# Kernel tuning notes

Measured on AMD Instinct MI355X. Metric: run time of the kernel, lower is better.

The kernel has to match this reference:

```python
import jax, jax.numpy as jnp
import numpy as np

L2_REG = 0.01  # config['l2_reg']


def setup_inputs() -> dict:
    key = jax.random.key(0)
    k1, k2, k3, k4 = jax.random.split(key, 4)
    N = 16384
    risk_pred = jax.random.normal(k1, (N, 1), dtype=jnp.float32)
    y = jax.random.uniform(k2, (N, 1), dtype=jnp.float32)  # survival times
    e = jax.random.randint(k3, (N, 1), 0, 2, dtype=jnp.int32)  # event indicator
    W = jax.random.normal(k4, (512, 256), dtype=jnp.float32)  # model weight for L2 reg
    return {"risk_pred": risk_pred, "y": y, "e": e, "W": W}


def reference(risk_pred, y, e, W):
    # mask[i, j] = 1 if y[j] <= y[i] else 0  (torch: mask[y.T - y > 0] = 0)
    mask = (y.T - y <= 0).astype(risk_pred.dtype)  # (N, N)
    exp_r = jnp.exp(risk_pred)                      # (N, 1), broadcasts over rows
    num = jnp.sum(exp_r * mask, axis=0)             # (N,) risk-set weighted sum per column
    den = jnp.sum(mask, axis=0)                     # (N,) risk-set size per column
    log_loss = jnp.log(num / den).reshape(-1, 1)    # (N, 1)
    ef = e.astype(risk_pred.dtype)
    neg_log_loss = -jnp.sum((risk_pred - log_loss) * ef) / jnp.sum(ef)
    l2_loss = L2_REG * jnp.linalg.norm(W)           # Regularization(order=2)
    return neg_log_loss + l2_loss
```

## Files before the change

kernel.cpp:

```cpp
#include <hip/hip_runtime.h>

#define L2_REG 0.01f
#define NTOT 16384
#define K    8
#define NBL  4096
#define GB   (K * NBL)
#define CAP  3072
#define NT   1024


__global__ __launch_bounds__(NT) void cox_sort(const float* __restrict__ rp,
                                               const float* __restrict__ y,
                                               const int* __restrict__ e,
                                               const float* __restrict__ W,
                                               float2* __restrict__ g_ye,
                                               int* __restrict__ pub_n,
                                               float* __restrict__ pub_S,
                                               float* __restrict__ pub_w,
                                               float* __restrict__ acc,
                                               int* __restrict__ cnt2) {
    __shared__ __align__(16) float2 s_ye[CAP];
    __shared__ __align__(16) int    s_off[NBL];
    __shared__ int   s_isc[16];
    __shared__ float s_f1[16], s_f2[16];

    const int t = threadIdx.x, wg = blockIdx.x;
    const int lane = t & 63, wave = t >> 6;

    *reinterpret_cast<int4*>(&s_off[4 * t]) = make_int4(0, 0, 0, 0);

    float yv[16], rk[16];
    {
        const float4* y4 = reinterpret_cast<const float4*>(y);
        const float4* r4 = reinterpret_cast<const float4*>(rp);
        const int4*   e4 = reinterpret_cast<const int4*>(e);
#pragma unroll
        for (int k = 0; k < 4; ++k) {
            const float4 yy = y4[k * NT + t];
            const float4 rr = r4[k * NT + t];
            const int4   ee = e4[k * NT + t];
            yv[4*k+0] = yy.x; yv[4*k+1] = yy.y; yv[4*k+2] = yy.z; yv[4*k+3] = yy.w;
            rk[4*k+0] = __int_as_float((__float_as_int(rr.x) & ~1) | (ee.x & 1));
            rk[4*k+1] = __int_as_float((__float_as_int(rr.y) & ~1) | (ee.y & 1));
            rk[4*k+2] = __int_as_float((__float_as_int(rr.z) & ~1) | (ee.z & 1));
            rk[4*k+3] = __int_as_float((__float_as_int(rr.w) & ~1) | (ee.w & 1));
        }
    }
    float wsum = 0.f;
    {
        const float4* W4 = reinterpret_cast<const float4*>(W) + wg * 4096;
#pragma unroll
        for (int m = 0; m < 4; ++m) {
            const float4 w = W4[m * NT + t];
            wsum = fmaf(w.x, w.x, wsum); wsum = fmaf(w.y, w.y, wsum);
            wsum = fmaf(w.z, w.z, wsum); wsum = fmaf(w.w, w.w, wsum);
        }
    }
    __syncthreads();

    const int lo = wg * NBL;
    float sp = 0.f;
#pragma unroll
    for (int k = 0; k < 16; ++k) {
        int g = (int)(yv[k] * (float)GB);
        g = min(max(g, 0), GB - 1);
        const unsigned lb = (unsigned)(g - lo);
        if (lb < NBL) { atomicAdd(&s_off[lb], 1); sp += __expf(rk[k]); }
    }
#pragma unroll
    for (int o = 32; o; o >>= 1) {
        sp   += __shfl_down(sp,   o, 64);
        wsum += __shfl_down(wsum, o, 64);
    }
    if (lane == 0) { s_f1[wave] = sp; s_f2[wave] = wsum; }
    __syncthreads();

    const int4 c4 = *reinterpret_cast<const int4*>(&s_off[4 * t]);
    const int cs = c4.x + c4.y + c4.z + c4.w;
    int ci = cs;
#pragma unroll
    for (int o = 1; o < 64; o <<= 1) {
        const int p = __shfl_up(ci, o, 64);
        if (lane >= o) ci += p;
    }
    if (lane == 63) s_isc[wave] = ci;
    __syncthreads();
    if (t < 16) {
        int v = s_isc[t];
#pragma unroll
        for (int o = 1; o < 16; o <<= 1) {
            const int p = __shfl_up(v, o, 64);
            if (lane >= o) v += p;
        }
        s_isc[t] = v;
    }
    __syncthreads();
    {
        const int base = ci - cs + (wave ? s_isc[wave - 1] : 0);
        s_off[4*t+0] = base;
        s_off[4*t+1] = base + c4.x;
        s_off[4*t+2] = base + c4.x + c4.y;
        s_off[4*t+3] = base + c4.x + c4.y + c4.z;
    }
    __syncthreads();

#pragma unroll
    for (int k = 0; k < 16; ++k) {
        int g = (int)(yv[k] * (float)GB);
        g = min(max(g, 0), GB - 1);
        const unsigned lb = (unsigned)(g - lo);
        if (lb < NBL) {
            const int pos = atomicAdd(&s_off[lb], 1);
            if (pos < CAP) s_ye[pos] = make_float2(yv[k], rk[k]);
        }
    }
    __syncthreads();

    {
        int start = t ? s_off[4 * t - 1] : 0;
#pragma unroll
        for (int c = 0; c < 4; ++c) {
            const int k1 = s_off[4 * t + c];
            for (int i = start + 1; i < k1; ++i) {
                const float2 v = s_ye[i];
                int j = i - 1;
                while (j >= start && s_ye[j].x > v.x) { s_ye[j + 1] = s_ye[j]; --j; }
                s_ye[j + 1] = v;
            }
            start = k1;
        }
    }
    __syncthreads();

    const int n = min(s_isc[15], CAP);
    for (int p = t; p < n; p += NT) g_ye[wg * CAP + p] = s_ye[p];
    if (t == 0) {
        float S = 0.f, WS = 0.f;
#pragma unroll
        for (int w = 0; w < 16; ++w) { S += s_f1[w]; WS += s_f2[w]; }
        pub_n[wg] = n; pub_S[wg] = S; pub_w[wg] = WS;
        if (wg == 0) { acc[0] = 0.f; acc[1] = 0.f; cnt2[0] = 0; }
    }
}

__global__ __launch_bounds__(NT) void cox_terms(const float2* __restrict__ g_ye,
                                                const int* __restrict__ pub_n,
                                                const float* __restrict__ pub_S,
                                                const float* __restrict__ pub_w,
                                                float* __restrict__ acc,
                                                int* __restrict__ cnt2,
                                                float* __restrict__ out) {
    __shared__ int   s_n[K];
    __shared__ float s_S[K];
    __shared__ float s_sc[16], s_r0[16], s_r1[16];

    const int t = threadIdx.x, wg = blockIdx.x;
    const int lane = t & 63, wave = t >> 6;

    if (t < K) { s_n[t] = pub_n[t]; s_S[t] = pub_S[t]; }
    __syncthreads();
    int off = 0; float suf = 0.f;
#pragma unroll
    for (int k = 0; k < K; ++k) {
        if (k < wg) off += s_n[k];
        if (k > wg) suf += s_S[k];
    }
    const int n = s_n[wg];
    const float2* chunk = g_ye + wg * CAP;

    float rv[3], ei[3];
    float csum = 0.f;
#pragma unroll
    for (int j = 0; j < 3; ++j) {
        const int p = 3 * t + j;
        rv[j] = 0.f; ei[j] = 0.f;
        if (p < n) { const float2 v = chunk[p]; rv[j] = v.y; ei[j] = __expf(v.y); csum += ei[j]; }
    }
    float s = csum;
#pragma unroll
    for (int o = 1; o < 64; o <<= 1) {
        const float v = __shfl_down(s, o, 64);
        if (lane + o < 64) s += v;
    }
    if (lane == 0) s_sc[wave] = s;
    __syncthreads();
    if (t < 16) {
        float v = s_sc[t];
#pragma unroll
        for (int o = 1; o < 16; o <<= 1) {
            const float p = __shfl_down(v, o, 64);
            if (t + o < 16) v += p;
        }
        s_sc[t] = v;
    }
    __syncthreads();
    float run = (s - csum) + ((wave < 15) ? s_sc[wave + 1] : 0.f) + suf;
    float term = 0.f, ecnt = 0.f;
#pragma unroll
    for (int j = 2; j >= 0; --j) {
        const int p = 3 * t + j;
        if (p < n) {
            run += ei[j];
            if (__float_as_int(rv[j]) & 1) {
                term += rv[j] - __logf(__fdividef(run, (float)(NTOT - (off + p))));
                ecnt += 1.f;
            }
        }
    }
#pragma unroll
    for (int o = 32; o; o >>= 1) {
        term += __shfl_down(term, o, 64);
        ecnt += __shfl_down(ecnt, o, 64);
    }
    if (lane == 0) { s_r0[wave] = term; s_r1[wave] = ecnt; }
    __syncthreads();
    if (t == 0) {
        float T = 0.f, E = 0.f;
#pragma unroll
        for (int w = 0; w < 16; ++w) { T += s_r0[w]; E += s_r1[w]; }
        atomicAdd(&acc[0], T);
        atomicAdd(&acc[1], E);
        __threadfence();
        if (atomicAdd(cnt2, 1) == K - 1) {
            const float a0 = atomicAdd(&acc[0], 0.f);
            const float a1 = atomicAdd(&acc[1], 0.f);
            float WS = 0.f;
#pragma unroll
            for (int k = 0; k < K; ++k) WS += pub_w[k];
            out[0] = -a0 / a1 + L2_REG * sqrtf(WS);
        }
    }
}

extern "C" void kernel_launch(void* const* d_in, const int* in_sizes, int n_in,
                              void* d_out, int out_size, void* d_ws, size_t ws_size,
                              hipStream_t stream) {
    (void)in_sizes; (void)n_in; (void)out_size; (void)ws_size;
    const float* rp = (const float*)d_in[0];
    const float* y  = (const float*)d_in[1];
    const int*   e  = (const int*)d_in[2];
    const float* W  = (const float*)d_in[3];

    float2* g_ye  = (float2*)d_ws;
    int*    pub_n = (int*)(g_ye + K * CAP);
    float*  pub_S = (float*)(pub_n + K);
    float*  pub_w = pub_S + K;
    float*  acc   = pub_w + K;
    int*    cnt2  = (int*)(acc + 2);

    cox_sort<<<dim3(K), dim3(NT), 0, stream>>>(rp, y, e, W, g_ye,
                                               pub_n, pub_S, pub_w, acc, cnt2);
    cox_terms<<<dim3(K), dim3(NT), 0, stream>>>(g_ye, pub_n, pub_S, pub_w,
                                                acc, cnt2, (float*)d_out);
}
```

Measured before the change: 72.51 us.

## Fuse per-block risk-set terms into sort kernel using local global-rank counts

Each block now counts how many samples fall in lower buckets and sums exp(risk) over higher buckets itself, which removes the dependency on other blocks' published counts and suffix sums. The per-block term computation then runs directly from shared memory inside the sort kernel, with no write and re-read of sorted chunks in global memory. The atomic last-block finalisation is replaced by a tiny single-wave reduction kernel. Each block redundantly scans all 16K elements for the prefix count and suffix sum, but it already loaded them all, so that costs little.

```diff
diff --git a/kernel.cpp b/kernel.cpp
--- a/kernel.cpp
+++ b/kernel.cpp
@@ -13,16 +13,18 @@
                                                const float* __restrict__ y,
                                                const int* __restrict__ e,
                                                const float* __restrict__ W,
-                                               float2* __restrict__ g_ye,
-                                               int* __restrict__ pub_n,
-                                               float* __restrict__ pub_S,
-                                               float* __restrict__ pub_w,
-                                               float* __restrict__ acc,
-                                               int* __restrict__ cnt2) {
+                                               float* __restrict__ pubT,
+                                               float* __restrict__ pubE,
+                                               float* __restrict__ pubW) {
     __shared__ __align__(16) float2 s_ye[CAP];
     __shared__ __align__(16) int    s_off[NBL];
     __shared__ int   s_isc[16];
+    __shared__ int   s_i1[16];
     __shared__ float s_f1[16], s_f2[16];
+    __shared__ float s_sc[16];
+    __shared__ float s_r0[16], s_r1[16];
+    __shared__ int   s_OFF;
+    __shared__ float s_SUF, s_WS;
 
     const int t = threadIdx.x, wg = blockIdx.x;
     const int lane = t & 63, wave = t >> 6;
@@ -30,6 +32,7 @@
     *reinterpret_cast<int4*>(&s_off[4 * t]) = make_int4(0, 0, 0, 0);
 
     float yv[16], rk[16];
+    int   bv[16];
     {
         const float4* y4 = reinterpret_cast<const float4*>(y);
         const float4* r4 = reinterpret_cast<const float4*>(rp);
@@ -46,6 +49,11 @@
             rk[4*k+3] = __int_as_float((__float_as_int(rr.w) & ~1) | (ee.w & 1));
         }
     }
+#pragma unroll
+    for (int k = 0; k < 16; ++k) {
+        int g = (int)(yv[k] * (float)GB);
+        bv[k] = min(max(g, 0), GB - 1);
+    }
     float wsum = 0.f;
     {
         const float4* W4 = reinterpret_cast<const float4*>(W) + wg * 4096;
@@ -58,21 +66,24 @@
     }
     __syncthreads();
 
-    const int lo = wg * NBL;
-    float sp = 0.f;
+    const int lo = wg * NBL, hi = lo + NBL;
+    int   bl = 0;
+    float hs = 0.f;
 #pragma unroll
     for (int k = 0; k < 16; ++k) {
-        int g = (int)(yv[k] * (float)GB);
-        g = min(max(g, 0), GB - 1);
-        const unsigned lb = (unsigned)(g - lo);
-        if (lb < NBL) { atomicAdd(&s_off[lb], 1); sp += __expf(rk[k]); }
+        const unsigned lb = (unsigned)(bv[k] - lo);
+        if (lb < NBL) atomicAdd(&s_off[lb], 1);
+        bl += (bv[k] < lo) ? 1 : 0;
+        const float ex = __expf(rk[k]);
+        hs = fmaf((bv[k] >= hi) ? 1.f : 0.f, ex, hs);
     }
 #pragma unroll
     for (int o = 32; o; o >>= 1) {
-        sp   += __shfl_down(sp,   o, 64);
+        bl   += __shfl_down(bl,   o, 64);
+        hs   += __shfl_down(hs,   o, 64);
         wsum += __shfl_down(wsum, o, 64);
     }
-    if (lane == 0) { s_f1[wave] = sp; s_f2[wave] = wsum; }
+    if (lane == 0) { s_i1[wave] = bl; s_f1[wave] = hs; s_f2[wave] = wsum; }
     __syncthreads();
 
     const int4 c4 = *reinterpret_cast<const int4*>(&s_off[4 * t]);
@@ -93,6 +104,12 @@
             if (lane >= o) v += p;
         }
         s_isc[t] = v;
+    }
+    if (t == 64) {
+        int   O = 0; float S = 0.f, Wp = 0.f;
+#pragma unroll
+        for (int w = 0; w < 16; ++w) { O += s_i1[w]; S += s_f1[w]; Wp += s_f2[w]; }
+        s_OFF = O; s_SUF = S; s_WS = Wp;
     }
     __syncthreads();
     {
@@ -106,9 +123,7 @@
 
 #pragma unroll
     for (int k = 0; k < 16; ++k) {
-        int g = (int)(yv[k] * (float)GB);
-        g = min(max(g, 0), GB - 1);
-        const unsigned lb = (unsigned)(g - lo);
+        const unsigned lb = (unsigned)(bv[k] - lo);
         if (lb < NBL) {
             const int pos = atomicAdd(&s_off[lb], 1);
             if (pos < CAP) s_ye[pos] = make_float2(yv[k], rk[k]);
@@ -133,48 +148,14 @@
     __syncthreads();
 
     const int n = min(s_isc[15], CAP);
-    for (int p = t; p < n; p += NT) g_ye[wg * CAP + p] = s_ye[p];
-    if (t == 0) {
-        float S = 0.f, WS = 0.f;
-#pragma unroll
-        for (int w = 0; w < 16; ++w) { S += s_f1[w]; WS += s_f2[w]; }
-        pub_n[wg] = n; pub_S[wg] = S; pub_w[wg] = WS;
-        if (wg == 0) { acc[0] = 0.f; acc[1] = 0.f; cnt2[0] = 0; }
-    }
-}
-
-__global__ __launch_bounds__(NT) void cox_terms(const float2* __restrict__ g_ye,
-                                                const int* __restrict__ pub_n,
-                                                const float* __restrict__ pub_S,
-                                                const float* __restrict__ pub_w,
-                                                float* __restrict__ acc,
-                                                int* __restrict__ cnt2,
-                                                float* __restrict__ out) {
-    __shared__ int   s_n[K];
-    __shared__ float s_S[K];
-    __shared__ float s_sc[16], s_r0[16], s_r1[16];
-
-    const int t = threadIdx.x, wg = blockIdx.x;
-    const int lane = t & 63, wave = t >> 6;
-
-    if (t < K) { s_n[t] = pub_n[t]; s_S[t] = pub_S[t]; }
-    __syncthreads();
-    int off = 0; float suf = 0.f;
-#pragma unroll
-    for (int k = 0; k < K; ++k) {
-        if (k < wg) off += s_n[k];
-        if (k > wg) suf += s_S[k];
-    }
-    const int n = s_n[wg];
-    const float2* chunk = g_ye + wg * CAP;
-
+    const int OFF = s_OFF;
     float rv[3], ei[3];
     float csum = 0.f;
 #pragma unroll
     for (int j = 0; j < 3; ++j) {
         const int p = 3 * t + j;
         rv[j] = 0.f; ei[j] = 0.f;
-        if (p < n) { const float2 v = chunk[p]; rv[j] = v.y; ei[j] = __expf(v.y); csum += ei[j]; }
+        if (p < n) { const float2 v = s_ye[p]; rv[j] = v.y; ei[j] = __expf(v.y); csum += ei[j]; }
     }
     float s = csum;
 #pragma unroll
@@ -194,7 +175,7 @@
         s_sc[t] = v;
     }
     __syncthreads();
-    float run = (s - csum) + ((wave < 15) ? s_sc[wave + 1] : 0.f) + suf;
+    float run = (s - csum) + ((wave < 15) ? s_sc[wave + 1] : 0.f) + s_SUF;
     float term = 0.f, ecnt = 0.f;
 #pragma unroll
     for (int j = 2; j >= 0; --j) {
@@ -202,7 +183,7 @@
         if (p < n) {
             run += ei[j];
             if (__float_as_int(rv[j]) & 1) {
-                term += rv[j] - __logf(__fdividef(run, (float)(NTOT - (off + p))));
+                term += rv[j] - __logf(__fdividef(run, (float)(NTOT - (OFF + p))));
                 ecnt += 1.f;
             }
         }
@@ -218,38 +199,38 @@
         float T = 0.f, E = 0.f;
 #pragma unroll
         for (int w = 0; w < 16; ++w) { T += s_r0[w]; E += s_r1[w]; }
-        atomicAdd(&acc[0], T);
-        atomicAdd(&acc[1], E);
-        __threadfence();
-        if (atomicAdd(cnt2, 1) == K - 1) {
-            const float a0 = atomicAdd(&acc[0], 0.f);
-            const float a1 = atomicAdd(&acc[1], 0.f);
-            float WS = 0.f;
-#pragma unroll
-            for (int k = 0; k < K; ++k) WS += pub_w[k];
-            out[0] = -a0 / a1 + L2_REG * sqrtf(WS);
-        }
-    }
+        pubT[wg] = T; pubE[wg] = E; pubW[wg] = s_WS;
+    }
+}
+
+__global__ __launch_bounds__(64) void cox_fin(const float* __restrict__ pubT,
+                                              const float* __restrict__ pubE,
+                                              const float* __restrict__ pubW,
+                                              float* __restrict__ out) {
+    const int t = threadIdx.x;
+    float T = 0.f, E = 0.f, WS = 0.f;
+    if (t < K) { T = pubT[t]; E = pubE[t]; WS = pubW[t]; }
+#pragma unroll
+    for (int o = 4; o; o >>= 1) {
+        T  += __shfl_down(T,  o, 64);
+        E  += __shfl_down(E,  o, 64);
+        WS += __shfl_down(WS, o, 64);
+    }
+    if (t == 0) out[0] = -T / E + L2_REG * sqrtf(WS);
 }
 
 extern "C" void kernel_launch(void* const* d_in, const int* in_sizes, int n_in,
                               void* d_out, int out_size, void* d_ws, size_t ws_size,
                               hipStream_t stream) {
     (void)in_sizes; (void)n_in; (void)out_size; (void)ws_size;
-    const float* rp = (const float*)d_in[0];
-    const float* y  = (const float*)d_in[1];
-    const int*   e  = (const int*)d_in[2];
-    const float* W  = (const float*)d_in[3];
-
-    float2* g_ye  = (float2*)d_ws;
-    int*    pub_n = (int*)(g_ye + K * CAP);
-    float*  pub_S = (float*)(pub_n + K);
-    float*  pub_w = pub_S + K;
-    float*  acc   = pub_w + K;
-    int*    cnt2  = (int*)(acc + 2);
-
-    cox_sort<<<dim3(K), dim3(NT), 0, stream>>>(rp, y, e, W, g_ye,
-                                               pub_n, pub_S, pub_w, acc, cnt2);
-    cox_terms<<<dim3(K), dim3(NT), 0, stream>>>(g_ye, pub_n, pub_S, pub_w,
-                                                acc, cnt2, (float*)d_out);
+    float* pubT = (float*)d_ws;
+    float* pubE = pubT + K;
+    float* pubW = pubE + K;
+
+    cox_sort<<<dim3(K), dim3(NT), 0, stream>>>((const float*)d_in[0],
+                                               (const float*)d_in[1],
+                                               (const int*)d_in[2],
+                                               (const float*)d_in[3],
+                                               pubT, pubE, pubW);
+    cox_fin<<<dim3(1), dim3(64), 0, stream>>>(pubT, pubE, pubW, (float*)d_out);
 }
```

Result: no change. 72.16 us (-0.5%).
